# Kernel optimization log

Hardware: AMD Instinct MI355X
Metric: run time of the kernel (lower is better)

Reference implementation:

```python
import jax, jax.numpy as jnp
import numpy as np
import math

B, SQ, SK, D = 32, 2048, 2048, 64


def setup_inputs() -> dict:
    key = jax.random.key(0)
    kq, kk, kv, km = jax.random.split(key, 4)
    Q = jax.random.normal(kq, (B, SQ, D), dtype=jnp.float32)
    K = jax.random.normal(kk, (B, SK, D), dtype=jnp.float32)
    V = jax.random.normal(kv, (B, SK, D), dtype=jnp.float32)
    mask = jax.random.randint(km, (B, SQ, SK), 0, 2) > 0  # bool, True = keep
    return {"Q": Q, "K": K, "V": V, "mask": mask}


def reference(Q, K, V, mask):
    dim_qk = Q.shape[-1]
    # [B, Sq, Sk] = Q @ K^T / sqrt(d)
    attn_score = jnp.einsum("bqd,bkd->bqk", Q, K) / math.sqrt(dim_qk)
    attn_score = jnp.where(mask, attn_score, jnp.float32(-1e9))
    attn_score = jax.nn.softmax(attn_score, axis=-1)
    output = jnp.einsum("bqk,bkd->bqd", attn_score, V)
    return (attn_score, output)
```

## Files before the change

### kernel.cpp

```cpp
#include <hip/hip_runtime.h>
#include <math.h>

#define NB 32
#define SQL 2048
#define SKL 2048
#define DH 64
#define EPITCH (SKL + 8)

typedef __attribute__((ext_vector_type(8))) short short8;
typedef __attribute__((ext_vector_type(4))) float f32x4;

__device__ __forceinline__ unsigned short f2bf(float f) {
    unsigned int u = __float_as_uint(f);
    u += 0x7FFFu + ((u >> 16) & 1u);
    return (unsigned short)(u >> 16);
}
__device__ __forceinline__ float bf2f(unsigned short h) {
    return __uint_as_float(((unsigned int)h) << 16);
}

__global__ __launch_bounds__(256)
void cvt_bf16_kernel(const float* __restrict__ in, unsigned short* __restrict__ out, int n4)
{
    const int i = blockIdx.x * 256 + threadIdx.x;
    if (i < n4) {
        const float4 v = reinterpret_cast<const float4*>(in)[i];
        ushort4 o;
        o.x = f2bf(v.x); o.y = f2bf(v.y); o.z = f2bf(v.z); o.w = f2bf(v.w);
        reinterpret_cast<ushort4*>(out)[i] = o;
    }
}

__global__ __launch_bounds__(256)
void vtrans_kernel(const float* __restrict__ V, unsigned short* __restrict__ Vt)
{
    __shared__ float tile[64][65];
    const int b  = blockIdx.x >> 5;
    const int kt = blockIdx.x & 31;
    const int t  = threadIdx.x;
    const int c4 = (t & 15) << 2;
    const int r0 = t >> 4;
    const float* vb = V + ((size_t)b * SKL + (size_t)kt * 64) * DH;
#pragma unroll
    for (int i = 0; i < 4; ++i) {
        const int r = r0 + i * 16;
        const float4 v = *reinterpret_cast<const float4*>(vb + (size_t)r * DH + c4);
        tile[r][c4] = v.x; tile[r][c4 + 1] = v.y; tile[r][c4 + 2] = v.z; tile[r][c4 + 3] = v.w;
    }
    __syncthreads();
    unsigned short* ob = Vt + (size_t)b * DH * SKL + (size_t)kt * 64;
#pragma unroll
    for (int i = 0; i < 4; ++i) {
        const int d = r0 + i * 16;
        ushort4 o;
        o.x = f2bf(tile[c4 + 0][d]);
        o.y = f2bf(tile[c4 + 1][d]);
        o.z = f2bf(tile[c4 + 2][d]);
        o.w = f2bf(tile[c4 + 3][d]);
        *reinterpret_cast<ushort4*>(ob + (size_t)d * SKL + c4) = o;
    }
}

__global__ __launch_bounds__(512, 4)
void sdpa_mfma_kernel(const unsigned short* __restrict__ Qb,
                      const unsigned short* __restrict__ Kb,
                      const unsigned short* __restrict__ Vtb,
                      const int* __restrict__ Mp,
                      float* __restrict__ Pout, float* __restrict__ Oout)
{
    __shared__ unsigned short e_sh[16 * EPITCH];
    __shared__ float l_part[8][16];
    __shared__ float inv_l[16];
    __shared__ f32x4 o_red[4 * 64];

    const int tid  = threadIdx.x;
    const int w    = tid >> 6;
    const int lane = tid & 63;
    const int quad = lane >> 4;
    const int s    = lane & 15;
    const int blk  = blockIdx.x;
    const int b    = blk >> 7;
    const int qt   = blk & 127;
    const int g0   = (b << 11) + (qt << 4);

    const unsigned short* qrow = Qb + (size_t)(g0 + s) * DH + quad * 8;
    const short8 aq0 = *reinterpret_cast<const short8*>(qrow);
    const short8 aq1 = *reinterpret_cast<const short8*>(qrow + 32);

    const size_t kvb = (size_t)b * SKL * DH;

    float l_acc = 0.f;
#pragma unroll 4
    for (int nt = 0; nt < 16; ++nt) {
        const int j0 = nt * 128 + w * 16;
        const unsigned short* kb = Kb + kvb + (size_t)(j0 + s) * DH + quad * 8;
        const short8 bk0 = *reinterpret_cast<const short8*>(kb);
        const short8 bk1 = *reinterpret_cast<const short8*>(kb + 32);

        f32x4 c = {0.f, 0.f, 0.f, 0.f};
        c = __builtin_amdgcn_mfma_f32_16x16x32_bf16(bk0, aq0, c, 0, 0, 0);
        c = __builtin_amdgcn_mfma_f32_16x16x32_bf16(bk1, aq1, c, 0, 0, 0);

        const int4 mk = *reinterpret_cast<const int4*>(
            Mp + (size_t)(g0 + s) * SKL + j0 + quad * 4);
        const float e0 = mk.x ? exp2f(c[0] * 0.18033688011112042f) : 0.0f;
        const float e1 = mk.y ? exp2f(c[1] * 0.18033688011112042f) : 0.0f;
        const float e2 = mk.z ? exp2f(c[2] * 0.18033688011112042f) : 0.0f;
        const float e3 = mk.w ? exp2f(c[3] * 0.18033688011112042f) : 0.0f;
        l_acc += (e0 + e1) + (e2 + e3);

        uint2 ev;
        ev.x = (unsigned int)f2bf(e0) | ((unsigned int)f2bf(e1) << 16);
        ev.y = (unsigned int)f2bf(e2) | ((unsigned int)f2bf(e3) << 16);
        *reinterpret_cast<uint2*>(&e_sh[s * EPITCH + j0 + quad * 4]) = ev;
    }

    l_acc += __shfl_xor(l_acc, 16, 64);
    l_acc += __shfl_xor(l_acc, 32, 64);
    if (lane < 16)
        l_part[w][lane] = l_acc;
    __syncthreads();
    if (tid < 16) {
        float t = 0.f;
#pragma unroll
        for (int wv = 0; wv < 8; ++wv) t += l_part[wv][tid];
        inv_l[tid] = 1.0f / t;
    }
    __syncthreads();

    float* pb = Pout + (size_t)g0 * SKL;
#pragma unroll 4
    for (int i = tid; i < 16 * (SKL / 4); i += 512) {
        const int row = i >> 9;
        const int c4  = (i & 511) << 2;
        const unsigned long long ev =
            *reinterpret_cast<const unsigned long long*>(&e_sh[row * EPITCH + c4]);
        const float il = inv_l[row];
        float4 pv;
        pv.x = bf2f((unsigned short)(ev))       * il;
        pv.y = bf2f((unsigned short)(ev >> 16)) * il;
        pv.z = bf2f((unsigned short)(ev >> 32)) * il;
        pv.w = bf2f((unsigned short)(ev >> 48)) * il;
        *reinterpret_cast<float4*>(pb + (size_t)row * SKL + c4) = pv;
    }

    f32x4 oacc = {0.f, 0.f, 0.f, 0.f};
    const int d0 = (w & 3) * 16;
    const int h  = w >> 2;
    const unsigned short* vtr = Vtb + (size_t)b * DH * SKL + (size_t)(d0 + s) * SKL;
#pragma unroll 4
    for (int kt = h * 32; kt < h * 32 + 32; ++kt) {
        const int k0 = kt * 32 + quad * 8;
        const short8 ap =
            *reinterpret_cast<const short8*>(&e_sh[s * EPITCH + k0]);
        const short8 bv = *reinterpret_cast<const short8*>(vtr + k0);
        oacc = __builtin_amdgcn_mfma_f32_16x16x32_bf16(ap, bv, oacc, 0, 0, 0);
    }
    if (w >= 4)
        o_red[(w - 4) * 64 + lane] = oacc;
    __syncthreads();
    if (w < 4) {
        const f32x4 o2 = o_red[w * 64 + lane];
#pragma unroll
        for (int r = 0; r < 4; ++r) {
            const int m = quad * 4 + r;
            Oout[(size_t)(g0 + m) * DH + d0 + s] = (oacc[r] + o2[r]) * inv_l[m];
        }
    }
}

extern "C" void kernel_launch(void* const* d_in, const int* in_sizes, int n_in,
                              void* d_out, int out_size, void* d_ws, size_t ws_size,
                              hipStream_t stream) {
    const float* Q = (const float*)d_in[0];
    const float* K = (const float*)d_in[1];
    const float* V = (const float*)d_in[2];
    const int*   M = (const int*)d_in[3];

    float* Pout = (float*)d_out;
    float* Oout = Pout + (size_t)NB * SQL * SKL;

    unsigned short* Qb = (unsigned short*)d_ws;
    unsigned short* Kb = Qb + (size_t)NB * SQL * DH;
    unsigned short* Vt = Kb + (size_t)NB * SKL * DH;

    const int n4q = NB * SQL * DH / 4;
    cvt_bf16_kernel<<<n4q / 256, 256, 0, stream>>>(Q, Qb, n4q);
    cvt_bf16_kernel<<<n4q / 256, 256, 0, stream>>>(K, Kb, n4q);
    vtrans_kernel<<<NB * 32, 256, 0, stream>>>(V, Vt);

    const int blocks = NB * (SQL / 16);
    sdpa_mfma_kernel<<<blocks, 512, 0, stream>>>(Qb, Kb, Vt, M, Pout, Oout);
}
```

Baseline: 1.077 ms.

## Pre-pack the int32 attention mask into bitmasks before the main attention kernel

A new pre-pass kernel turns each int32 mask row into 64 packed 32-bit words, using wave ballots, in a layout matched to the per-wave, per-tile access pattern of the attention kernel. The attention kernel then loads 16 mask words per lane once, up front, and tests bits instead of issuing strided int4 mask loads inside the score loop. That loop is also unrolled further. This moves the large mask read into a simple streaming kernel and takes global-load latency out of the MFMA/exp loop. The cost is an extra launch, a small extra write and read of the packed mask, and more registers per lane.

```diff
diff --git a/kernel.cpp b/kernel.cpp
--- a/kernel.cpp
+++ b/kernel.cpp
@@ -61,11 +61,34 @@
     }
 }
 
+__global__ __launch_bounds__(256)
+void maskbits_kernel(const int* __restrict__ M, unsigned int* __restrict__ Mb)
+{
+    __shared__ unsigned int words[64];
+    const int r = blockIdx.x;
+    const int t = threadIdx.x;
+    const int v = t >> 6, lane = t & 63;
+    const int* mr = M + (size_t)r * SKL;
+#pragma unroll
+    for (int j = 0; j < 8; ++j) {
+        const int c1 = v * 512 + j * 64;
+        const unsigned long long bal = __ballot(mr[c1 + lane] != 0);
+        if (lane == 0) {
+            const int c2 = c1 + 32;
+            words[((c1 >> 5) & 3) * 16 + (c1 >> 7)] = (unsigned int)bal;
+            words[((c2 >> 5) & 3) * 16 + (c2 >> 7)] = (unsigned int)(bal >> 32);
+        }
+    }
+    __syncthreads();
+    if (t < 64)
+        Mb[(size_t)r * 64 + t] = words[t];
+}
+
 __global__ __launch_bounds__(512, 4)
 void sdpa_mfma_kernel(const unsigned short* __restrict__ Qb,
                       const unsigned short* __restrict__ Kb,
                       const unsigned short* __restrict__ Vtb,
-                      const int* __restrict__ Mp,
+                      const unsigned int* __restrict__ Mb,
                       float* __restrict__ Pout, float* __restrict__ Oout)
 {
     __shared__ unsigned short e_sh[16 * EPITCH];
@@ -87,10 +110,20 @@
     const short8 aq0 = *reinterpret_cast<const short8*>(qrow);
     const short8 aq1 = *reinterpret_cast<const short8*>(qrow + 32);
 
+    unsigned int mword[16];
+    {
+        const unsigned int* mbase = Mb + (size_t)(g0 + s) * 64 + (w >> 1) * 16;
+        *reinterpret_cast<uint4*>(&mword[0])  = *reinterpret_cast<const uint4*>(mbase);
+        *reinterpret_cast<uint4*>(&mword[4])  = *reinterpret_cast<const uint4*>(mbase + 4);
+        *reinterpret_cast<uint4*>(&mword[8])  = *reinterpret_cast<const uint4*>(mbase + 8);
+        *reinterpret_cast<uint4*>(&mword[12]) = *reinterpret_cast<const uint4*>(mbase + 12);
+    }
+    const int mshift = ((w & 1) << 4) + (quad << 2);
+
     const size_t kvb = (size_t)b * SKL * DH;
 
     float l_acc = 0.f;
-#pragma unroll 4
+#pragma unroll 8
     for (int nt = 0; nt < 16; ++nt) {
         const int j0 = nt * 128 + w * 16;
         const unsigned short* kb = Kb + kvb + (size_t)(j0 + s) * DH + quad * 8;
@@ -101,12 +134,11 @@
         c = __builtin_amdgcn_mfma_f32_16x16x32_bf16(bk0, aq0, c, 0, 0, 0);
         c = __builtin_amdgcn_mfma_f32_16x16x32_bf16(bk1, aq1, c, 0, 0, 0);
 
-        const int4 mk = *reinterpret_cast<const int4*>(
-            Mp + (size_t)(g0 + s) * SKL + j0 + quad * 4);
-        const float e0 = mk.x ? exp2f(c[0] * 0.18033688011112042f) : 0.0f;
-        const float e1 = mk.y ? exp2f(c[1] * 0.18033688011112042f) : 0.0f;
-        const float e2 = mk.z ? exp2f(c[2] * 0.18033688011112042f) : 0.0f;
-        const float e3 = mk.w ? exp2f(c[3] * 0.18033688011112042f) : 0.0f;
+        const unsigned int mw = mword[nt] >> mshift;
+        const float e0 = (mw & 1u) ? exp2f(c[0] * 0.18033688011112042f) : 0.0f;
+        const float e1 = (mw & 2u) ? exp2f(c[1] * 0.18033688011112042f) : 0.0f;
+        const float e2 = (mw & 4u) ? exp2f(c[2] * 0.18033688011112042f) : 0.0f;
+        const float e3 = (mw & 8u) ? exp2f(c[3] * 0.18033688011112042f) : 0.0f;
         l_acc += (e0 + e1) + (e2 + e3);
 
         uint2 ev;
@@ -183,12 +215,14 @@
     unsigned short* Qb = (unsigned short*)d_ws;
     unsigned short* Kb = Qb + (size_t)NB * SQL * DH;
     unsigned short* Vt = Kb + (size_t)NB * SKL * DH;
+    unsigned int*   Mb = (unsigned int*)(Vt + (size_t)NB * SKL * DH);
 
     const int n4q = NB * SQL * DH / 4;
     cvt_bf16_kernel<<<n4q / 256, 256, 0, stream>>>(Q, Qb, n4q);
     cvt_bf16_kernel<<<n4q / 256, 256, 0, stream>>>(K, Kb, n4q);
     vtrans_kernel<<<NB * 32, 256, 0, stream>>>(V, Vt);
+    maskbits_kernel<<<NB * SQL, 256, 0, stream>>>(M, Mb);
 
     const int blocks = NB * (SQL / 16);
-    sdpa_mfma_kernel<<<blocks, 512, 0, stream>>>(Qb, Kb, Vt, M, Pout, Oout);
-}
+    sdpa_mfma_kernel<<<blocks, 512, 0, stream>>>(Qb, Kb, Vt, Mb, Pout, Oout);
+}
```

New measurement: 1.253 ms. +16.3%, slower.

## Recompute QK^T in second pass, drop full-row LDS buffer, fuse PV per tile

Applied to the files above, without the earlier changes.

The kernel no longer stages a 16x2048 bf16 exp buffer in LDS. It makes two passes over K. The first computes the row sums and packs the mask into bits kept in registers. The second recomputes the scores, writes the normalized probabilities straight to global with nontemporal stores, and accumulates P·V per 32-key tile through a small per-wave LDS scratch. The block shrinks to 256 threads with higher occupancy, and the partial outputs are reduced across 4 waves. This trades twice the QK MFMA and K loads for far less LDS use, better occupancy, and a mask read only once.

```diff
diff --git a/kernel.cpp b/kernel.cpp
--- a/kernel.cpp
+++ b/kernel.cpp
@@ -5,18 +5,18 @@
 #define SQL 2048
 #define SKL 2048
 #define DH 64
-#define EPITCH (SKL + 8)
+#define EWP 40
+#define SC 0.18033688011112042f
 
 typedef __attribute__((ext_vector_type(8))) short short8;
 typedef __attribute__((ext_vector_type(4))) float f32x4;
+typedef __attribute__((ext_vector_type(4))) int   i32x4;
+typedef __attribute__((ext_vector_type(2))) unsigned int u32x2;
 
 __device__ __forceinline__ unsigned short f2bf(float f) {
     unsigned int u = __float_as_uint(f);
     u += 0x7FFFu + ((u >> 16) & 1u);
     return (unsigned short)(u >> 16);
-}
-__device__ __forceinline__ float bf2f(unsigned short h) {
-    return __uint_as_float(((unsigned int)h) << 16);
 }
 
 __global__ __launch_bounds__(256)
@@ -61,26 +61,24 @@
     }
 }
 
-__global__ __launch_bounds__(512, 4)
+__global__ __launch_bounds__(256, 6)
 void sdpa_mfma_kernel(const unsigned short* __restrict__ Qb,
                       const unsigned short* __restrict__ Kb,
                       const unsigned short* __restrict__ Vtb,
                       const int* __restrict__ Mp,
                       float* __restrict__ Pout, float* __restrict__ Oout)
 {
-    __shared__ unsigned short e_sh[16 * EPITCH];
-    __shared__ float l_part[8][16];
+    __shared__ float ored[4][16][68];
+    __shared__ float l_part[4][16];
     __shared__ float inv_l[16];
-    __shared__ f32x4 o_red[4 * 64];
 
     const int tid  = threadIdx.x;
     const int w    = tid >> 6;
     const int lane = tid & 63;
     const int quad = lane >> 4;
     const int s    = lane & 15;
-    const int blk  = blockIdx.x;
-    const int b    = blk >> 7;
-    const int qt   = blk & 127;
+    const int b    = blockIdx.x >> 7;
+    const int qt   = blockIdx.x & 127;
     const int g0   = (b << 11) + (qt << 4);
 
     const unsigned short* qrow = Qb + (size_t)(g0 + s) * DH + quad * 8;
@@ -88,31 +86,47 @@
     const short8 aq1 = *reinterpret_cast<const short8*>(qrow + 32);
 
     const size_t kvb = (size_t)b * SKL * DH;
-
+    const int* mrow = Mp + (size_t)(g0 + s) * SKL;
+
+    unsigned int mregs[4] = {0u, 0u, 0u, 0u};
     float l_acc = 0.f;
-#pragma unroll 4
-    for (int nt = 0; nt < 16; ++nt) {
-        const int j0 = nt * 128 + w * 16;
-        const unsigned short* kb = Kb + kvb + (size_t)(j0 + s) * DH + quad * 8;
-        const short8 bk0 = *reinterpret_cast<const short8*>(kb);
-        const short8 bk1 = *reinterpret_cast<const short8*>(kb + 32);
-
-        f32x4 c = {0.f, 0.f, 0.f, 0.f};
-        c = __builtin_amdgcn_mfma_f32_16x16x32_bf16(bk0, aq0, c, 0, 0, 0);
-        c = __builtin_amdgcn_mfma_f32_16x16x32_bf16(bk1, aq1, c, 0, 0, 0);
-
-        const int4 mk = *reinterpret_cast<const int4*>(
-            Mp + (size_t)(g0 + s) * SKL + j0 + quad * 4);
-        const float e0 = mk.x ? exp2f(c[0] * 0.18033688011112042f) : 0.0f;
-        const float e1 = mk.y ? exp2f(c[1] * 0.18033688011112042f) : 0.0f;
-        const float e2 = mk.z ? exp2f(c[2] * 0.18033688011112042f) : 0.0f;
-        const float e3 = mk.w ? exp2f(c[3] * 0.18033688011112042f) : 0.0f;
-        l_acc += (e0 + e1) + (e2 + e3);
-
-        uint2 ev;
-        ev.x = (unsigned int)f2bf(e0) | ((unsigned int)f2bf(e1) << 16);
-        ev.y = (unsigned int)f2bf(e2) | ((unsigned int)f2bf(e3) << 16);
-        *reinterpret_cast<uint2*>(&e_sh[s * EPITCH + j0 + quad * 4]) = ev;
+
+#pragma unroll 1
+    for (int it = 0; it < 4; ++it) {
+#pragma unroll
+        for (int o = 0; o < 4; ++o) {
+            const int nt = it * 4 + o;
+            const int j0 = nt * 128 + w * 32;
+            const unsigned short* kb0 = Kb + kvb + (size_t)(j0 + s) * DH + quad * 8;
+            const short8 k0a = *reinterpret_cast<const short8*>(kb0);
+            const short8 k0b = *reinterpret_cast<const short8*>(kb0 + 32);
+            const short8 k1a = *reinterpret_cast<const short8*>(kb0 + 16 * DH);
+            const short8 k1b = *reinterpret_cast<const short8*>(kb0 + 16 * DH + 32);
+            f32x4 c0 = {0.f, 0.f, 0.f, 0.f}, c1 = {0.f, 0.f, 0.f, 0.f};
+            c0 = __builtin_amdgcn_mfma_f32_16x16x32_bf16(k0a, aq0, c0, 0, 0, 0);
+            c0 = __builtin_amdgcn_mfma_f32_16x16x32_bf16(k0b, aq1, c0, 0, 0, 0);
+            c1 = __builtin_amdgcn_mfma_f32_16x16x32_bf16(k1a, aq0, c1, 0, 0, 0);
+            c1 = __builtin_amdgcn_mfma_f32_16x16x32_bf16(k1b, aq1, c1, 0, 0, 0);
+
+            const i32x4 m0 = __builtin_nontemporal_load(
+                reinterpret_cast<const i32x4*>(mrow + j0 + quad * 4));
+            const i32x4 m1 = __builtin_nontemporal_load(
+                reinterpret_cast<const i32x4*>(mrow + j0 + 16 + quad * 4));
+            const unsigned int bits =
+                (m0.x ? 1u : 0u)  | (m0.y ? 2u : 0u)  | (m0.z ? 4u : 0u)   | (m0.w ? 8u : 0u) |
+                (m1.x ? 16u : 0u) | (m1.y ? 32u : 0u) | (m1.z ? 64u : 0u)  | (m1.w ? 128u : 0u);
+            mregs[o] |= bits << (it * 8);
+
+            float e;
+            e = (bits & 1u)   ? exp2f(c0[0] * SC) : 0.f; l_acc += e;
+            e = (bits & 2u)   ? exp2f(c0[1] * SC) : 0.f; l_acc += e;
+            e = (bits & 4u)   ? exp2f(c0[2] * SC) : 0.f; l_acc += e;
+            e = (bits & 8u)   ? exp2f(c0[3] * SC) : 0.f; l_acc += e;
+            e = (bits & 16u)  ? exp2f(c1[0] * SC) : 0.f; l_acc += e;
+            e = (bits & 32u)  ? exp2f(c1[1] * SC) : 0.f; l_acc += e;
+            e = (bits & 64u)  ? exp2f(c1[2] * SC) : 0.f; l_acc += e;
+            e = (bits & 128u) ? exp2f(c1[3] * SC) : 0.f; l_acc += e;
+        }
     }
 
     l_acc += __shfl_xor(l_acc, 16, 64);
@@ -120,52 +134,93 @@
     if (lane < 16)
         l_part[w][lane] = l_acc;
     __syncthreads();
-    if (tid < 16) {
-        float t = 0.f;
-#pragma unroll
-        for (int wv = 0; wv < 8; ++wv) t += l_part[wv][tid];
-        inv_l[tid] = 1.0f / t;
-    }
-    __syncthreads();
-
-    float* pb = Pout + (size_t)g0 * SKL;
-#pragma unroll 4
-    for (int i = tid; i < 16 * (SKL / 4); i += 512) {
-        const int row = i >> 9;
-        const int c4  = (i & 511) << 2;
-        const unsigned long long ev =
-            *reinterpret_cast<const unsigned long long*>(&e_sh[row * EPITCH + c4]);
-        const float il = inv_l[row];
-        float4 pv;
-        pv.x = bf2f((unsigned short)(ev))       * il;
-        pv.y = bf2f((unsigned short)(ev >> 16)) * il;
-        pv.z = bf2f((unsigned short)(ev >> 32)) * il;
-        pv.w = bf2f((unsigned short)(ev >> 48)) * il;
-        *reinterpret_cast<float4*>(pb + (size_t)row * SKL + c4) = pv;
-    }
-
-    f32x4 oacc = {0.f, 0.f, 0.f, 0.f};
-    const int d0 = (w & 3) * 16;
-    const int h  = w >> 2;
-    const unsigned short* vtr = Vtb + (size_t)b * DH * SKL + (size_t)(d0 + s) * SKL;
-#pragma unroll 4
-    for (int kt = h * 32; kt < h * 32 + 32; ++kt) {
-        const int k0 = kt * 32 + quad * 8;
-        const short8 ap =
-            *reinterpret_cast<const short8*>(&e_sh[s * EPITCH + k0]);
-        const short8 bv = *reinterpret_cast<const short8*>(vtr + k0);
-        oacc = __builtin_amdgcn_mfma_f32_16x16x32_bf16(ap, bv, oacc, 0, 0, 0);
-    }
-    if (w >= 4)
-        o_red[(w - 4) * 64 + lane] = oacc;
-    __syncthreads();
-    if (w < 4) {
-        const f32x4 o2 = o_red[w * 64 + lane];
-#pragma unroll
-        for (int r = 0; r < 4; ++r) {
-            const int m = quad * 4 + r;
-            Oout[(size_t)(g0 + m) * DH + d0 + s] = (oacc[r] + o2[r]) * inv_l[m];
+    if (tid < 16)
+        inv_l[tid] = 1.0f / (l_part[0][tid] + l_part[1][tid] +
+                             l_part[2][tid] + l_part[3][tid]);
+    __syncthreads();
+    const float il = inv_l[s];
+
+    unsigned short* eW = reinterpret_cast<unsigned short*>(&ored[0][0][0]) + w * 2176;
+
+    f32x4 o0 = {0.f, 0.f, 0.f, 0.f}, o1 = o0, o2 = o0, o3 = o0;
+    const unsigned short* vrow = Vtb + (size_t)b * DH * SKL + (size_t)s * SKL;
+
+#pragma unroll 1
+    for (int it = 0; it < 4; ++it) {
+#pragma unroll
+        for (int o = 0; o < 4; ++o) {
+            const int nt = it * 4 + o;
+            const int j0 = nt * 128 + w * 32;
+            const unsigned short* kb0 = Kb + kvb + (size_t)(j0 + s) * DH + quad * 8;
+            const short8 k0a = *reinterpret_cast<const short8*>(kb0);
+            const short8 k0b = *reinterpret_cast<const short8*>(kb0 + 32);
+            const short8 k1a = *reinterpret_cast<const short8*>(kb0 + 16 * DH);
+            const short8 k1b = *reinterpret_cast<const short8*>(kb0 + 16 * DH + 32);
+            f32x4 c0 = {0.f, 0.f, 0.f, 0.f}, c1 = {0.f, 0.f, 0.f, 0.f};
+            c0 = __builtin_amdgcn_mfma_f32_16x16x32_bf16(k0a, aq0, c0, 0, 0, 0);
+            c0 = __builtin_amdgcn_mfma_f32_16x16x32_bf16(k0b, aq1, c0, 0, 0, 0);
+            c1 = __builtin_amdgcn_mfma_f32_16x16x32_bf16(k1a, aq0, c1, 0, 0, 0);
+            c1 = __builtin_amdgcn_mfma_f32_16x16x32_bf16(k1b, aq1, c1, 0, 0, 0);
+
+            const unsigned int bits = mregs[o] >> (it * 8);
+            const float e00 = (bits & 1u)   ? exp2f(c0[0] * SC) : 0.f;
+            const float e01 = (bits & 2u)   ? exp2f(c0[1] * SC) : 0.f;
+            const float e02 = (bits & 4u)   ? exp2f(c0[2] * SC) : 0.f;
+            const float e03 = (bits & 8u)   ? exp2f(c0[3] * SC) : 0.f;
+            const float e10 = (bits & 16u)  ? exp2f(c1[0] * SC) : 0.f;
+            const float e11 = (bits & 32u)  ? exp2f(c1[1] * SC) : 0.f;
+            const float e12 = (bits & 64u)  ? exp2f(c1[2] * SC) : 0.f;
+            const float e13 = (bits & 128u) ? exp2f(c1[3] * SC) : 0.f;
+
+            float* pb = Pout + (size_t)(g0 + s) * SKL + j0 + quad * 4;
+            const f32x4 p0 = {e00 * il, e01 * il, e02 * il, e03 * il};
+            const f32x4 p1 = {e10 * il, e11 * il, e12 * il, e13 * il};
+            __builtin_nontemporal_store(p0, reinterpret_cast<f32x4*>(pb));
+            __builtin_nontemporal_store(p1, reinterpret_cast<f32x4*>(pb + 16));
+
+            u32x2 ev0, ev1;
+            ev0.x = (unsigned)f2bf(e00) | ((unsigned)f2bf(e01) << 16);
+            ev0.y = (unsigned)f2bf(e02) | ((unsigned)f2bf(e03) << 16);
+            ev1.x = (unsigned)f2bf(e10) | ((unsigned)f2bf(e11) << 16);
+            ev1.y = (unsigned)f2bf(e12) | ((unsigned)f2bf(e13) << 16);
+            *reinterpret_cast<u32x2*>(eW + s * EWP + quad * 4) = ev0;
+            *reinterpret_cast<u32x2*>(eW + s * EWP + 16 + quad * 4) = ev1;
+
+            const short8 ap = *reinterpret_cast<const short8*>(eW + s * EWP + quad * 8);
+            const unsigned short* vc = vrow + j0 + quad * 8;
+            o0 = __builtin_amdgcn_mfma_f32_16x16x32_bf16(
+                     ap, *reinterpret_cast<const short8*>(vc), o0, 0, 0, 0);
+            o1 = __builtin_amdgcn_mfma_f32_16x16x32_bf16(
+                     ap, *reinterpret_cast<const short8*>(vc + 16 * SKL), o1, 0, 0, 0);
+            o2 = __builtin_amdgcn_mfma_f32_16x16x32_bf16(
+                     ap, *reinterpret_cast<const short8*>(vc + 32 * SKL), o2, 0, 0, 0);
+            o3 = __builtin_amdgcn_mfma_f32_16x16x32_bf16(
+                     ap, *reinterpret_cast<const short8*>(vc + 48 * SKL), o3, 0, 0, 0);
         }
+    }
+
+#pragma unroll
+    for (int r = 0; r < 4; ++r) {
+        const int m = quad * 4 + r;
+        ored[w][m][s]      = o0[r];
+        ored[w][m][16 + s] = o1[r];
+        ored[w][m][32 + s] = o2[r];
+        ored[w][m][48 + s] = o3[r];
+    }
+    __syncthreads();
+    {
+        const int m  = tid >> 4;
+        const int d4 = (tid & 15) << 2;
+        const float* orp = &ored[0][m][d4];
+        f32x4 a0 = *reinterpret_cast<const f32x4*>(orp);
+        f32x4 a1 = *reinterpret_cast<const f32x4*>(orp + 16 * 68);
+        f32x4 a2 = *reinterpret_cast<const f32x4*>(orp + 32 * 68);
+        f32x4 a3 = *reinterpret_cast<const f32x4*>(orp + 48 * 68);
+        f32x4 r = (a0 + a1) + (a2 + a3);
+        const float ilm = inv_l[m];
+        r[0] *= ilm; r[1] *= ilm; r[2] *= ilm; r[3] *= ilm;
+        __builtin_nontemporal_store(r,
+            reinterpret_cast<f32x4*>(Oout + (size_t)(g0 + m) * DH + d4));
     }
 }
 
@@ -190,5 +245,5 @@
     vtrans_kernel<<<NB * 32, 256, 0, stream>>>(V, Vt);
 
     const int blocks = NB * (SQL / 16);
-    sdpa_mfma_kernel<<<blocks, 512, 0, stream>>>(Qb, Kb, Vt, M, Pout, Oout);
-}
+    sdpa_mfma_kernel<<<blocks, 256, 0, stream>>>(Qb, Kb, Vt, M, Pout, Oout);
+}
```

Result: slower. 1.214 ms (+12.7%).

## Double block size to 1024 threads with contiguous per-wave column chunks

Applied to the files above, without the earlier changes.

Launches 1024-thread blocks so each of 16 waves handles a contiguous 128-column slice of the score row, and splits the PV reduction four ways over K instead of two. The cross-wave output reduction reuses the score LDS buffer instead of a separate array. This aims to put more waves in flight per CU to hide mask reads and probability writes. The aggressive launch bounds may constrain registers.

```diff
diff --git a/kernel.cpp b/kernel.cpp
--- a/kernel.cpp
+++ b/kernel.cpp
@@ -5,10 +5,13 @@
 #define SQL 2048
 #define SKL 2048
 #define DH 64
-#define EPITCH (SKL + 8)
+#define EPITCH 2056
+#define SC 0.18033688011112042f
 
 typedef __attribute__((ext_vector_type(8))) short short8;
 typedef __attribute__((ext_vector_type(4))) float f32x4;
+typedef __attribute__((ext_vector_type(4))) int   i32x4;
+typedef __attribute__((ext_vector_type(2))) unsigned int u32x2;
 
 __device__ __forceinline__ unsigned short f2bf(float f) {
     unsigned int u = __float_as_uint(f);
@@ -61,26 +64,24 @@
     }
 }
 
-__global__ __launch_bounds__(512, 4)
+__global__ __launch_bounds__(1024, 8)
 void sdpa_mfma_kernel(const unsigned short* __restrict__ Qb,
                       const unsigned short* __restrict__ Kb,
                       const unsigned short* __restrict__ Vtb,
                       const int* __restrict__ Mp,
                       float* __restrict__ Pout, float* __restrict__ Oout)
 {
-    __shared__ unsigned short e_sh[16 * EPITCH];
-    __shared__ float l_part[8][16];
+    __shared__ __align__(16) unsigned short e_sh[16 * EPITCH];
+    __shared__ float l_part[16][16];
     __shared__ float inv_l[16];
-    __shared__ f32x4 o_red[4 * 64];
 
     const int tid  = threadIdx.x;
     const int w    = tid >> 6;
     const int lane = tid & 63;
     const int quad = lane >> 4;
     const int s    = lane & 15;
-    const int blk  = blockIdx.x;
-    const int b    = blk >> 7;
-    const int qt   = blk & 127;
+    const int b    = blockIdx.x >> 7;
+    const int qt   = blockIdx.x & 127;
     const int g0   = (b << 11) + (qt << 4);
 
     const unsigned short* qrow = Qb + (size_t)(g0 + s) * DH + quad * 8;
@@ -88,12 +89,13 @@
     const short8 aq1 = *reinterpret_cast<const short8*>(qrow + 32);
 
     const size_t kvb = (size_t)b * SKL * DH;
+    const int* mrow = Mp + (size_t)(g0 + s) * SKL;
 
     float l_acc = 0.f;
-#pragma unroll 4
-    for (int nt = 0; nt < 16; ++nt) {
-        const int j0 = nt * 128 + w * 16;
-        const unsigned short* kb = Kb + kvb + (size_t)(j0 + s) * DH + quad * 8;
+#pragma unroll
+    for (int i = 0; i < 8; ++i) {
+        const int col0 = w * 128 + i * 16;
+        const unsigned short* kb = Kb + kvb + (size_t)(col0 + s) * DH + quad * 8;
         const short8 bk0 = *reinterpret_cast<const short8*>(kb);
         const short8 bk1 = *reinterpret_cast<const short8*>(kb + 32);
 
@@ -101,18 +103,17 @@
         c = __builtin_amdgcn_mfma_f32_16x16x32_bf16(bk0, aq0, c, 0, 0, 0);
         c = __builtin_amdgcn_mfma_f32_16x16x32_bf16(bk1, aq1, c, 0, 0, 0);
 
-        const int4 mk = *reinterpret_cast<const int4*>(
-            Mp + (size_t)(g0 + s) * SKL + j0 + quad * 4);
-        const float e0 = mk.x ? exp2f(c[0] * 0.18033688011112042f) : 0.0f;
-        const float e1 = mk.y ? exp2f(c[1] * 0.18033688011112042f) : 0.0f;
-        const float e2 = mk.z ? exp2f(c[2] * 0.18033688011112042f) : 0.0f;
-        const float e3 = mk.w ? exp2f(c[3] * 0.18033688011112042f) : 0.0f;
+        const i32x4 mk = *reinterpret_cast<const i32x4*>(mrow + col0 + quad * 4);
+        const float e0 = mk.x ? exp2f(c[0] * SC) : 0.f;
+        const float e1 = mk.y ? exp2f(c[1] * SC) : 0.f;
+        const float e2 = mk.z ? exp2f(c[2] * SC) : 0.f;
+        const float e3 = mk.w ? exp2f(c[3] * SC) : 0.f;
         l_acc += (e0 + e1) + (e2 + e3);
 
-        uint2 ev;
-        ev.x = (unsigned int)f2bf(e0) | ((unsigned int)f2bf(e1) << 16);
-        ev.y = (unsigned int)f2bf(e2) | ((unsigned int)f2bf(e3) << 16);
-        *reinterpret_cast<uint2*>(&e_sh[s * EPITCH + j0 + quad * 4]) = ev;
+        u32x2 ev;
+        ev.x = (unsigned)f2bf(e0) | ((unsigned)f2bf(e1) << 16);
+        ev.y = (unsigned)f2bf(e2) | ((unsigned)f2bf(e3) << 16);
+        *reinterpret_cast<u32x2*>(&e_sh[s * EPITCH + col0 + quad * 4]) = ev;
     }
 
     l_acc += __shfl_xor(l_acc, 16, 64);
@@ -123,49 +124,54 @@
     if (tid < 16) {
         float t = 0.f;
 #pragma unroll
-        for (int wv = 0; wv < 8; ++wv) t += l_part[wv][tid];
+        for (int wv = 0; wv < 16; ++wv) t += l_part[wv][tid];
         inv_l[tid] = 1.0f / t;
     }
     __syncthreads();
 
     float* pb = Pout + (size_t)g0 * SKL;
-#pragma unroll 4
-    for (int i = tid; i < 16 * (SKL / 4); i += 512) {
-        const int row = i >> 9;
-        const int c4  = (i & 511) << 2;
+#pragma unroll
+    for (int i = 0; i < 8; ++i) {
+        const int idx = i * 1024 + tid;
+        const int row = idx >> 9;
+        const int c4  = (idx & 511) << 2;
         const unsigned long long ev =
             *reinterpret_cast<const unsigned long long*>(&e_sh[row * EPITCH + c4]);
         const float il = inv_l[row];
-        float4 pv;
-        pv.x = bf2f((unsigned short)(ev))       * il;
-        pv.y = bf2f((unsigned short)(ev >> 16)) * il;
-        pv.z = bf2f((unsigned short)(ev >> 32)) * il;
-        pv.w = bf2f((unsigned short)(ev >> 48)) * il;
-        *reinterpret_cast<float4*>(pb + (size_t)row * SKL + c4) = pv;
+        f32x4 pv;
+        pv[0] = bf2f((unsigned short)(ev))       * il;
+        pv[1] = bf2f((unsigned short)(ev >> 16)) * il;
+        pv[2] = bf2f((unsigned short)(ev >> 32)) * il;
+        pv[3] = bf2f((unsigned short)(ev >> 48)) * il;
+        *reinterpret_cast<f32x4*>(pb + (size_t)row * SKL + c4) = pv;
     }
 
     f32x4 oacc = {0.f, 0.f, 0.f, 0.f};
     const int d0 = (w & 3) * 16;
-    const int h  = w >> 2;
-    const unsigned short* vtr = Vtb + (size_t)b * DH * SKL + (size_t)(d0 + s) * SKL;
+    const int kq = w >> 2;
+    const unsigned short* vtr =
+        Vtb + (size_t)b * DH * SKL + (size_t)(d0 + s) * SKL + kq * 512;
 #pragma unroll 4
-    for (int kt = h * 32; kt < h * 32 + 32; ++kt) {
-        const int k0 = kt * 32 + quad * 8;
+    for (int it = 0; it < 16; ++it) {
+        const int k0 = it * 32 + quad * 8;
         const short8 ap =
-            *reinterpret_cast<const short8*>(&e_sh[s * EPITCH + k0]);
+            *reinterpret_cast<const short8*>(&e_sh[s * EPITCH + kq * 512 + k0]);
         const short8 bv = *reinterpret_cast<const short8*>(vtr + k0);
         oacc = __builtin_amdgcn_mfma_f32_16x16x32_bf16(ap, bv, oacc, 0, 0, 0);
     }
-    if (w >= 4)
-        o_red[(w - 4) * 64 + lane] = oacc;
-    __syncthreads();
-    if (w < 4) {
-        const f32x4 o2 = o_red[w * 64 + lane];
-#pragma unroll
-        for (int r = 0; r < 4; ++r) {
-            const int m = quad * 4 + r;
-            Oout[(size_t)(g0 + m) * DH + d0 + s] = (oacc[r] + o2[r]) * inv_l[m];
-        }
+
+    __syncthreads();
+    float* op = reinterpret_cast<float*>(e_sh);
+#pragma unroll
+    for (int r = 0; r < 4; ++r)
+        op[kq * 1024 + (quad * 4 + r) * 64 + d0 + s] = oacc[r];
+    __syncthreads();
+    {
+        const int m = tid >> 6;
+        const int d = tid & 63;
+        const float o = op[m * 64 + d] + op[1024 + m * 64 + d] +
+                        op[2048 + m * 64 + d] + op[3072 + m * 64 + d];
+        Oout[(size_t)(g0 + m) * DH + d] = o * inv_l[m];
     }
 }
 
@@ -190,5 +196,5 @@
     vtrans_kernel<<<NB * 32, 256, 0, stream>>>(V, Vt);
 
     const int blocks = NB * (SQL / 16);
-    sdpa_mfma_kernel<<<blocks, 512, 0, stream>>>(Qb, Kb, Vt, M, Pout, Oout);
-}
+    sdpa_mfma_kernel<<<blocks, 1024, 0, stream>>>(Qb, Kb, Vt, M, Pout, Oout);
+}
```

New measurement: 1.078 ms. About the same (+0.1%).
